# Kernel optimization log

Measured on AMD Instinct MI355X. Metric: run time of the kernel, lower is better.

The kernel has to match this reference:

```python
import jax, jax.numpy as jnp
import numpy as np

B, K, W, H = 32, 64, 100, 150
ALPHA = 0.2        # leaky-relu slope
THRES = 2e-4       # causal threshold


def setup_inputs() -> dict:
    ks = jax.random.split(jax.random.key(0), 20)
    s = 0.1
    inp = {
        "x": jax.random.normal(ks[0], (B, K, W), jnp.float32),
        "y": jax.random.normal(ks[1], (B, K, 1), jnp.float32),
        "z_noise": jax.random.normal(ks[2], (B, H), jnp.float32),
        "lin_w": jax.random.normal(ks[3], (W, W), jnp.float32) * s,
        "lin_b": jax.random.normal(ks[4], (W,), jnp.float32) * s,
        "a": jax.random.normal(ks[5], (2, 1), jnp.float32),
        "bias": jax.random.normal(ks[6], (K, K * W), jnp.float32) * 0.01,
        "gl_wih": jax.random.normal(ks[7], (3 * H, W), jnp.float32) * s,
        "gl_whh": jax.random.normal(ks[8], (3 * H, H), jnp.float32) * s,
        "gl_bih": jax.random.normal(ks[9], (3 * H,), jnp.float32) * s,
        "gl_bhh": jax.random.normal(ks[10], (3 * H,), jnp.float32) * s,
        "mu_w": jax.random.normal(ks[11], (H, H), jnp.float32) * s,
        "mu_b": jax.random.normal(ks[12], (H,), jnp.float32) * s,
        "std_w": jax.random.normal(ks[13], (H, H), jnp.float32) * s,
        "std_b": jax.random.normal(ks[14], (H,), jnp.float32) * s,
        "net_wih": jax.random.normal(ks[15], (K, 3 * H, W), jnp.float32) * s,
        "net_whh": jax.random.normal(ks[16], (K, 3 * H, H), jnp.float32) * s,
        "net_bih": jax.random.normal(ks[17], (K, 3 * H), jnp.float32) * s,
        "net_bhh": jax.random.normal(ks[18], (K, 3 * H), jnp.float32) * s,
    }
    return inp


def _gru_last(wih, whh, bih, bhh, xs, h0):
    # xs: [B, S, in], h0: [B, H] -> final hidden [B, H]. PyTorch gate order r,z,n.
    gx = jnp.einsum('bsi,gi->sbg', xs, wih) + bih  # [S, B, 3H]
    h_dim = h0.shape[-1]

    def step(h, g):
        gh = h @ whh.T + bhh
        r = jax.nn.sigmoid(g[:, :h_dim] + gh[:, :h_dim])
        z = jax.nn.sigmoid(g[:, h_dim:2 * h_dim] + gh[:, h_dim:2 * h_dim])
        n = jnp.tanh(g[:, 2 * h_dim:] + r * gh[:, 2 * h_dim:])
        return (1.0 - z) * n + z * h, None

    h_last, _ = jax.lax.scan(step, h0, gx)
    return h_last


def reference(x, y, z_noise, lin_w, lin_b, a, bias, gl_wih, gl_whh, gl_bih, gl_bhh,
              mu_w, mu_b, std_w, std_b, net_wih, net_whh, net_bih, net_bhh):
    xw = x[:, :, -W:]
    Wx = xw @ lin_w.T + lin_b                       # [B, K, W]
    v = Wx.reshape(Wx.shape[0], K * W)              # [B, K*W]
    # e = a_input @ a, where a_input[...,0]=y broadcast, a_input[...,1]=v tiled per node
    e = a[0, 0] * y + a[1, 0] * v[:, None, :] + bias  # [B, K, K*W]
    e = jax.nn.leaky_relu(e, ALPHA)
    attention = jax.nn.softmax(e, axis=2)           # dropout p=0 -> identity
    A = attention >= THRES                           # [B, K, K*W] mask
    Ax = jnp.where(A, v[:, None, :], 0.0)
    cause_x = Wx + Ax.sum(axis=2, keepdims=True)    # [B, K, W]
    # left GRU over the node dimension (seq len = K)
    h0 = jnp.zeros((cause_x.shape[0], H), cause_x.dtype)
    h_t = _gru_last(gl_wih, gl_whh, gl_bih, gl_bhh, cause_x, h0)  # [B, H]
    mu = h_t @ mu_w.T + mu_b
    log_var = h_t @ std_w.T + std_b
    sigma = jnp.exp(0.5 * log_var)
    z = mu + sigma * z_noise                        # [B, H]
    # K independent GRUs, same input Wx and same init state z -> vmap over weights
    causes = jax.vmap(lambda wi, wh, bi, bh: _gru_last(wi, wh, bi, bh, Wx, z))(
        net_wih, net_whh, net_bih, net_bhh)         # [K, B, H]
    return causes.transpose(1, 0, 2)                # [B, K, H]
```

## Files before the change

### kernel.cpp

```cpp
#include <hip/hip_runtime.h>

#define Bc 32
#define Kc 64
#define Wc 100
#define Hc 150
#define H3c 450
#define KWc 6400
#define ALPHAc 0.2f
#define THRESc 0.0002f

typedef unsigned int u32;
typedef unsigned short u16;
typedef __attribute__((ext_vector_type(8))) short short8;
typedef __attribute__((ext_vector_type(4))) float floatx4;

#define OFF_WX      0u
#define OFF_CS      204800u
#define OFF_GX      206848u
#define OFF_HT      1128448u
#define OFF_Z       1133248u

__device__ __forceinline__ float us2f(u16 u){ u32 x=((u32)u)<<16; return __uint_as_float(x); }
__device__ __forceinline__ u16 f2us(float f){
  u32 x = __float_as_uint(f);
  u32 r = (x + 0x7fffu + ((x>>16)&1u)) >> 16;
  return (u16)r;
}

__global__ void wx_kernel(const float* __restrict__ x, const float* __restrict__ lin_w,
                          const float* __restrict__ lin_b, float* __restrict__ ws){
  int o = blockIdx.x*256 + threadIdx.x;
  if (o >= Bc*KWc) return;
  int i = o % Wc;
  int bk = o / Wc;
  const float4* xr = (const float4*)(x + bk*Wc);
  const float4* wr = (const float4*)(lin_w + i*Wc);
  float acc = lin_b[i];
  #pragma unroll
  for (int j=0;j<25;j++){
    float4 xv = xr[j], wv = wr[j];
    acc += xv.x*wv.x + xv.y*wv.y + xv.z*wv.z + xv.w*wv.w;
  }
  ws[OFF_WX + o] = acc;
}

__global__ void attn_kernel(const float* __restrict__ y, const float* __restrict__ a,
                            const float* __restrict__ bias, float* __restrict__ ws){
  __shared__ float e_l[KWc];
  __shared__ float red[4];
  int row = blockIdx.x;
  int b = row >> 6, k = row & 63;
  int tid = threadIdx.x;
  float a0 = a[0], a1 = a[1];
  float yv = y[row];
  const float* v = ws + OFF_WX + b*KWc;
  const float* br = bias + k*KWc;
  float m = -3.4e38f;
  for (int j=tid; j<KWc; j+=256){
    float e = a0*yv + a1*v[j] + br[j];
    e = (e >= 0.f) ? e : ALPHAc*e;
    e_l[j] = e;
    m = fmaxf(m, e);
  }
  for (int o=32;o;o>>=1) m = fmaxf(m, __shfl_down(m, o));
  if ((tid&63)==0) red[tid>>6] = m;
  __syncthreads();
  m = fmaxf(fmaxf(red[0],red[1]), fmaxf(red[2],red[3]));
  __syncthreads();
  float ssum = 0.f;
  for (int j=tid; j<KWc; j+=256){
    float ex = expf(e_l[j]-m);
    e_l[j] = ex;
    ssum += ex;
  }
  for (int o=32;o;o>>=1) ssum += __shfl_down(ssum, o);
  if ((tid&63)==0) red[tid>>6] = ssum;
  __syncthreads();
  float s = red[0]+red[1]+red[2]+red[3];
  __syncthreads();
  float cs = 0.f;
  for (int j=tid; j<KWc; j+=256){
    float att = e_l[j] / s;
    if (att >= THRESc) cs += v[j];
  }
  for (int o=32;o;o>>=1) cs += __shfl_down(cs, o);
  if ((tid&63)==0) red[tid>>6] = cs;
  __syncthreads();
  if (tid==0) ws[OFF_CS + row] = red[0]+red[1]+red[2]+red[3];
}

__global__ void glproj_kernel(const float* __restrict__ gl_wih, const float* __restrict__ gl_bih,
                              float* __restrict__ ws){
  int o = blockIdx.x*256 + threadIdx.x;
  if (o >= Kc*Bc*H3c) return;
  int g = o % H3c;
  int t = o / H3c;
  int b = t & 31, s = t >> 5;
  float cs = ws[OFF_CS + b*Kc + s];
  const float4* xr = (const float4*)(ws + OFF_WX + b*KWc + s*Wc);
  const float4* wr = (const float4*)(gl_wih + g*Wc);
  float acc = gl_bih[g];
  #pragma unroll
  for (int j=0;j<25;j++){
    float4 wv = wr[j], xv = xr[j];
    acc += (xv.x+cs)*wv.x + (xv.y+cs)*wv.y + (xv.z+cs)*wv.z + (xv.w+cs)*wv.w;
  }
  ws[OFF_GX + o] = acc;
}

__global__ void __launch_bounds__(512,1) glgru4_kernel(
    const float* __restrict__ gl_whh, const float* __restrict__ gl_bhh,
    float* __restrict__ ws){
  __shared__ __align__(16) u16 bF[10*16*40];
  __shared__ float g_l[480*10];
  int b0 = blockIdx.x*8;
  int tid = threadIdx.x;
  int w = tid >> 6, lane = tid & 63, quad = lane >> 4, n16 = lane & 15;

  short8 whhA[4][5];
  #pragma unroll
  for (int ti=0; ti<4; ti++){
    int tile = w*4 + ti;
    int sec = tile/10;
    int sr = (tile - sec*10)*16 + n16;
    bool rowok = (tile < 30) && (sr < Hc);
    int grow = sec*Hc + sr;
    #pragma unroll
    for (int c=0;c<5;c++){
      union { short8 v; u16 u[8]; } t8;
      #pragma unroll
      for (int j=0;j<8;j++){
        int k = c*32 + quad*8 + j;
        float v = (rowok && k < Hc) ? gl_whh[(size_t)grow*Hc + k] : 0.f;
        t8.u[j] = f2us(v);
      }
      whhA[ti][c] = t8.v;
    }
  }
  for (int i=tid; i<10*16*40/2; i+=512) ((u32*)bF)[i] = 0u;

  float hst[3] = {0.f,0.f,0.f};
  float bh_r[3], bh_z[3], bh_n[3];
  int tT[3], tBL[3];
  #pragma unroll
  for (int q=0;q<3;q++){
    int task = tid + q*512;
    if (task < 1200){
      int bl = task/150, t = task - bl*150;
      tT[q] = t; tBL[q] = bl;
      bh_r[q] = gl_bhh[t];
      bh_z[q] = gl_bhh[Hc+t];
      bh_n[q] = gl_bhh[2*Hc+t];
    } else { tT[q] = 0; tBL[q] = -1; }
  }

  for (int s=0;s<Kc;s++){
    __syncthreads();
    float gxr[3], gxz[3], gxn[3];
    const float* gxb = ws + OFF_GX + (size_t)(s*Bc)*H3c;
    #pragma unroll
    for (int q=0;q<3;q++){
      if (tBL[q] >= 0){
        const float* gp = gxb + (size_t)(b0+tBL[q])*H3c;
        int t = tT[q];
        gxr[q] = gp[t]; gxz[q] = gp[Hc+t]; gxn[q] = gp[2*Hc+t];
      }
    }
    const u16* bBase = bF + (size_t)n16*40 + (size_t)quad*8;
    short8 bh[10];
    #pragma unroll
    for (int c=0;c<10;c++) bh[c] = *(const short8*)(bBase + (size_t)c*640);
    floatx4 acc[4] = {{0.f,0.f,0.f,0.f},{0.f,0.f,0.f,0.f},{0.f,0.f,0.f,0.f},{0.f,0.f,0.f,0.f}};
    #pragma unroll
    for (int c=0;c<10;c++){
      int ca = (c<5)? c : (c-5);
      #pragma unroll
      for (int ti=0;ti<4;ti++)
        acc[ti] = __builtin_amdgcn_mfma_f32_16x16x32_bf16(whhA[ti][ca], bh[c], acc[ti], 0,0,0);
    }
    if (n16 < 8){
      #pragma unroll
      for (int ti=0;ti<4;ti++){
        int tile = w*4 + ti;
        if (tile < 30){
          int row0 = tile*16 + quad*4;
          float* gp = g_l + row0*10 + n16;
          #pragma unroll
          for (int r=0;r<4;r++) gp[r*10] = acc[ti][r];
        }
      }
    }
    __syncthreads();
    #pragma unroll
    for (int q=0;q<3;q++){
      if (tBL[q] >= 0){
        int t = tT[q], bl = tBL[q];
        float a_r = gxr[q] + g_l[t*10+bl] + bh_r[q];
        float a_z = gxz[q] + g_l[(160+t)*10+bl] + bh_z[q];
        float r  = 1.f/(1.f+__expf(-a_r));
        float zz = 1.f/(1.f+__expf(-a_z));
        float nx = gxn[q] + r*(g_l[(320+t)*10+bl] + bh_n[q]);
        nx = fminf(fmaxf(nx,-15.f),15.f);
        float e2 = __expf(2.f*nx);
        float n = (e2-1.f)/(e2+1.f);
        float h = (1.f-zz)*n + zz*hst[q];
        hst[q] = h;
        u16 hi = f2us(h); float hif = us2f(hi); u16 lo = f2us(h - hif);
        bF[(t>>5)*640 + bl*40 + (t&31)] = hi;
        bF[(5+(t>>5))*640 + bl*40 + (t&31)] = lo;
      }
    }
  }
  #pragma unroll
  for (int q=0;q<3;q++){
    if (tBL[q] >= 0)
      ws[OFF_HT + (size_t)(b0+tBL[q])*Hc + tT[q]] = hst[q];
  }
}

__global__ void z_kernel(const float* __restrict__ z_noise, const float* __restrict__ mu_w,
                         const float* __restrict__ mu_b, const float* __restrict__ std_w,
                         const float* __restrict__ std_b, float* __restrict__ ws){
  int o = blockIdx.x*256 + threadIdx.x;
  if (o >= Bc*Hc) return;
  int t = o % Hc, b = o / Hc;
  const float* h = ws + OFF_HT + b*Hc;
  const float2* mwr = (const float2*)(mu_w + t*Hc);
  const float2* swr = (const float2*)(std_w + t*Hc);
  float mu = mu_b[t], lv = std_b[t];
  for (int j=0;j<Hc/2;j++){
    float2 mw = mwr[j], sw = swr[j];
    float h0 = h[2*j], h1 = h[2*j+1];
    mu += h0*mw.x + h1*mw.y;
    lv += h0*sw.x + h1*sw.y;
  }
  float sg = expf(0.5f*lv);
  ws[OFF_Z + o] = mu + sg*z_noise[o];
}

__global__ void __launch_bounds__(512,1) causes3_kernel(
    const float* __restrict__ net_wih, const float* __restrict__ net_whh,
    const float* __restrict__ net_bih, const float* __restrict__ net_bhh,
    const float* __restrict__ ws, float* __restrict__ out){
  __shared__ __align__(16) u16 bF[14*16*40];
  __shared__ float g_rz[320*10];
  __shared__ float g_nh[160*10];
  __shared__ float g_np[160*10];
  int kk = blockIdx.x & 63, bg = blockIdx.x >> 6, b0 = bg*8;
  int tid = threadIdx.x;
  int w = tid >> 6, lane = tid & 63, quad = lane >> 4, n16 = lane & 15;
  const float* whhk = net_whh + (size_t)kk*H3c*Hc;
  const float* wihk = net_wih + (size_t)kk*H3c*Wc;
  const float* bihk = net_bih + kk*H3c;
  const float* bhhk = net_bhh + kk*H3c;

  short8 whhA[4][5], wihA[4][4];
  #pragma unroll
  for (int ti=0; ti<4; ti++){
    int tile = w*4 + ti;
    int sec = tile/10;
    int sr = (tile - sec*10)*16 + n16;
    bool rowok = (tile < 30) && (sr < Hc);
    int grow = sec*Hc + sr;
    #pragma unroll
    for (int c=0;c<5;c++){
      union { short8 v; u16 u[8]; } t8;
      #pragma unroll
      for (int j=0;j<8;j++){
        int k = c*32 + quad*8 + j;
        float v = (rowok && k < Hc) ? whhk[(size_t)grow*Hc + k] : 0.f;
        t8.u[j] = f2us(v);
      }
      whhA[ti][c] = t8.v;
    }
    #pragma unroll
    for (int c=0;c<4;c++){
      union { short8 v; u16 u[8]; } t8;
      #pragma unroll
      for (int j=0;j<8;j++){
        int k = c*32 + quad*8 + j;
        float v = (rowok && k < Wc) ? wihk[(size_t)grow*Wc + k] : 0.f;
        t8.u[j] = f2us(v);
      }
      wihA[ti][c] = t8.v;
    }
  }

  for (int i=tid; i<14*16*40/2; i+=512) ((u32*)bF)[i] = 0u;

  float hst[3] = {0.f,0.f,0.f};
  float brz_r[3], brz_z[3], bnh_[3], bnp_[3];
  #pragma unroll
  for (int q=0;q<3;q++){
    int task = tid + q*512;
    if (task < 1200){
      int t = task >> 3, bb = task & 7;
      float h = ws[OFF_Z + (b0+bb)*Hc + t];
      hst[q] = h;
      brz_r[q] = bhhk[t]      + bihk[t];
      brz_z[q] = bhhk[Hc+t]   + bihk[Hc+t];
      bnh_[q]  = bhhk[2*Hc+t];
      bnp_[q]  = bihk[2*Hc+t];
      u16 hi = f2us(h); float hif = us2f(hi); u16 lo = f2us(h - hif);
      bF[(t>>5)*640 + bb*40 + (t&31)] = hi;
      bF[(5+(t>>5))*640 + bb*40 + (t&31)] = lo;
    }
  }
  for (int it=tid; it<800; it+=512){
    int bb = it/100, i = it - bb*100;
    float xv = ws[OFF_WX + (b0+bb)*KWc + i];
    bF[(10+(i>>5))*640 + bb*40 + (i&31)] = f2us(xv);
  }

  int bb0 = tid/100, i0 = tid - bb0*100;
  int it1 = tid + 512;
  int bb1 = it1/100, i1 = it1 - bb1*100;
  bool v1ok = (it1 < 800);

  const bool isN = (w >= 5);
  for (int s=0;s<Kc;s++){
    float xp0 = 0.f, xp1 = 0.f;
    if (s < Kc-1){
      xp0 = ws[OFF_WX + (size_t)(b0+bb0)*KWc + (s+1)*Wc + i0];
      if (v1ok) xp1 = ws[OFF_WX + (size_t)(b0+bb1)*KWc + (s+1)*Wc + i1];
    }
    __syncthreads();
    const u16* bBase = bF + (size_t)n16*40 + (size_t)quad*8;
    short8 bx[4];
    #pragma unroll
    for (int c=0;c<4;c++) bx[c] = *(const short8*)(bBase + (size_t)(10+c)*640);
    floatx4 acc[4] = {{0.f,0.f,0.f,0.f},{0.f,0.f,0.f,0.f},{0.f,0.f,0.f,0.f},{0.f,0.f,0.f,0.f}};
    #pragma unroll
    for (int ca=0;ca<4;ca++){
      #pragma unroll
      for (int ti=0;ti<4;ti++)
        acc[ti] = __builtin_amdgcn_mfma_f32_16x16x32_bf16(wihA[ti][ca], bx[ca], acc[ti], 0,0,0);
    }
    short8 bh[10];
    #pragma unroll
    for (int c=0;c<10;c++) bh[c] = *(const short8*)(bBase + (size_t)c*640);
    if (isN){
      if (n16 < 8){
        #pragma unroll
        for (int ti=0;ti<4;ti++){
          int tile = w*4 + ti;
          if (tile < 30){
            int srb = (tile - 20)*16 + quad*4;
            float* gq = g_np + srb*10 + n16;
            #pragma unroll
            for (int r=0;r<4;r++) gq[r*10] = acc[ti][r];
          }
        }
      }
      #pragma unroll
      for (int ti=0;ti<4;ti++) acc[ti] = (floatx4){0.f,0.f,0.f,0.f};
    }
    #pragma unroll
    for (int c=0;c<10;c++){
      int ca = (c<5)? c : (c-5);
      #pragma unroll
      for (int ti=0;ti<4;ti++)
        acc[ti] = __builtin_amdgcn_mfma_f32_16x16x32_bf16(whhA[ti][ca], bh[c], acc[ti], 0,0,0);
    }
    if (n16 < 8){
      #pragma unroll
      for (int ti=0;ti<4;ti++){
        int tile = w*4 + ti;
        if (tile < 30){
          int sec = tile/10;
          int srb = (tile - sec*10)*16 + quad*4;
          if (sec < 2){
            float* gp = g_rz + (sec*160 + srb)*10 + n16;
            #pragma unroll
            for (int r=0;r<4;r++) gp[r*10] = acc[ti][r];
          } else {
            float* gh = g_nh + srb*10 + n16;
            #pragma unroll
            for (int r=0;r<4;r++) gh[r*10] = acc[ti][r];
          }
        }
      }
    }
    __syncthreads();
    #pragma unroll
    for (int q=0;q<3;q++){
      int task = tid + q*512;
      if (task < 1200){
        int t = task >> 3, bb = task & 7;
        float a_r = g_rz[t*10+bb] + brz_r[q];
        float a_z = g_rz[(160+t)*10+bb] + brz_z[q];
        float r  = 1.f/(1.f+__expf(-a_r));
        float zz = 1.f/(1.f+__expf(-a_z));
        float nx = (g_np[t*10+bb] + bnp_[q]) + r*(g_nh[t*10+bb] + bnh_[q]);
        nx = fminf(fmaxf(nx,-15.f),15.f);
        float e2 = __expf(2.f*nx);
        float n = (e2-1.f)/(e2+1.f);
        float h = (1.f-zz)*n + zz*hst[q];
        hst[q] = h;
        u16 hi = f2us(h); float hif = us2f(hi); u16 lo = f2us(h - hif);
        bF[(t>>5)*640 + bb*40 + (t&31)] = hi;
        bF[(5+(t>>5))*640 + bb*40 + (t&31)] = lo;
      }
    }
    if (s < Kc-1){
      bF[(10+(i0>>5))*640 + bb0*40 + (i0&31)] = f2us(xp0);
      if (v1ok) bF[(10+(i1>>5))*640 + bb1*40 + (i1&31)] = f2us(xp1);
    }
  }
  #pragma unroll
  for (int q=0;q<3;q++){
    int task = tid + q*512;
    if (task < 1200){
      int t = task >> 3, bb = task & 7;
      out[((size_t)(b0+bb)*Kc + kk)*Hc + t] = hst[q];
    }
  }
}

extern "C" void kernel_launch(void* const* d_in, const int* in_sizes, int n_in,
                              void* d_out, int out_size, void* d_ws, size_t ws_size,
                              hipStream_t stream){
  const float* x        = (const float*)d_in[0];
  const float* y        = (const float*)d_in[1];
  const float* z_noise  = (const float*)d_in[2];
  const float* lin_w    = (const float*)d_in[3];
  const float* lin_b    = (const float*)d_in[4];
  const float* a        = (const float*)d_in[5];
  const float* bias     = (const float*)d_in[6];
  const float* gl_wih   = (const float*)d_in[7];
  const float* gl_whh   = (const float*)d_in[8];
  const float* gl_bih   = (const float*)d_in[9];
  const float* gl_bhh   = (const float*)d_in[10];
  const float* mu_w     = (const float*)d_in[11];
  const float* mu_b     = (const float*)d_in[12];
  const float* std_w    = (const float*)d_in[13];
  const float* std_b    = (const float*)d_in[14];
  const float* net_wih  = (const float*)d_in[15];
  const float* net_whh  = (const float*)d_in[16];
  const float* net_bih  = (const float*)d_in[17];
  const float* net_bhh  = (const float*)d_in[18];
  float* ws = (float*)d_ws;
  float* out = (float*)d_out;

  wx_kernel<<<(Bc*KWc+255)/256, 256, 0, stream>>>(x, lin_w, lin_b, ws);
  attn_kernel<<<Bc*Kc, 256, 0, stream>>>(y, a, bias, ws);
  glproj_kernel<<<(Kc*Bc*H3c+255)/256, 256, 0, stream>>>(gl_wih, gl_bih, ws);
  glgru4_kernel<<<4, 512, 0, stream>>>(gl_whh, gl_bhh, ws);
  z_kernel<<<(Bc*Hc+255)/256, 256, 0, stream>>>(z_noise, mu_w, mu_b, std_w, std_b, ws);
  causes3_kernel<<<Kc*4, 512, 0, stream>>>(net_wih, net_whh, net_bih, net_bhh, ws, out);
}
```

Before: 516.6 us.

## Vectorize attention softmax, use log-space threshold, batch LDS reads in GRU steps

The attention kernel now reads inputs as float4, uses fast __expf, and compares logits against m+log(THRES*s) instead of dividing every element, which drops one LDS write pass and a barrier. Weight loads into the MFMA fragments use float2 reads, and the GRU gate updates first gather all shared-memory values and then compute, to expose more memory-level parallelism. In the net GRU loop the load of the next input is moved after the barrier. The log-space threshold and __expf can flip mask decisions for values near the threshold.

```diff
diff --git a/kernel.cpp b/kernel.cpp
--- a/kernel.cpp
+++ b/kernel.cpp
@@ -46,21 +46,27 @@
 
 __global__ void attn_kernel(const float* __restrict__ y, const float* __restrict__ a,
                             const float* __restrict__ bias, float* __restrict__ ws){
-  __shared__ float e_l[KWc];
+  __shared__ __align__(16) float e_l[KWc];
   __shared__ float red[4];
   int row = blockIdx.x;
   int b = row >> 6, k = row & 63;
   int tid = threadIdx.x;
   float a0 = a[0], a1 = a[1];
   float yv = y[row];
-  const float* v = ws + OFF_WX + b*KWc;
-  const float* br = bias + k*KWc;
+  const float4* v4  = (const float4*)(ws + OFF_WX + (size_t)b*KWc);
+  const float4* br4 = (const float4*)(bias + (size_t)k*KWc);
+  float4* e4 = (float4*)e_l;
+  float ay = a0*yv;
   float m = -3.4e38f;
-  for (int j=tid; j<KWc; j+=256){
-    float e = a0*yv + a1*v[j] + br[j];
-    e = (e >= 0.f) ? e : ALPHAc*e;
-    e_l[j] = e;
-    m = fmaxf(m, e);
+  for (int j=tid; j<KWc/4; j+=256){
+    float4 vv = v4[j], bb = br4[j];
+    float4 e;
+    e.x = ay + a1*vv.x + bb.x; e.x = (e.x>=0.f)?e.x:ALPHAc*e.x;
+    e.y = ay + a1*vv.y + bb.y; e.y = (e.y>=0.f)?e.y:ALPHAc*e.y;
+    e.z = ay + a1*vv.z + bb.z; e.z = (e.z>=0.f)?e.z:ALPHAc*e.z;
+    e.w = ay + a1*vv.w + bb.w; e.w = (e.w>=0.f)?e.w:ALPHAc*e.w;
+    e4[j] = e;
+    m = fmaxf(m, fmaxf(fmaxf(e.x,e.y), fmaxf(e.z,e.w)));
   }
   for (int o=32;o;o>>=1) m = fmaxf(m, __shfl_down(m, o));
   if ((tid&63)==0) red[tid>>6] = m;
@@ -68,20 +74,23 @@
   m = fmaxf(fmaxf(red[0],red[1]), fmaxf(red[2],red[3]));
   __syncthreads();
   float ssum = 0.f;
-  for (int j=tid; j<KWc; j+=256){
-    float ex = expf(e_l[j]-m);
-    e_l[j] = ex;
-    ssum += ex;
+  for (int j=tid; j<KWc/4; j+=256){
+    float4 e = e4[j];
+    ssum += __expf(e.x-m) + __expf(e.y-m) + __expf(e.z-m) + __expf(e.w-m);
   }
   for (int o=32;o;o>>=1) ssum += __shfl_down(ssum, o);
   if ((tid&63)==0) red[tid>>6] = ssum;
   __syncthreads();
   float s = red[0]+red[1]+red[2]+red[3];
-  __syncthreads();
+  float thr = m + logf(THRESc * s);
   float cs = 0.f;
-  for (int j=tid; j<KWc; j+=256){
-    float att = e_l[j] / s;
-    if (att >= THRESc) cs += v[j];
+  for (int j=tid; j<KWc/4; j+=256){
+    float4 e = e4[j];
+    float4 vv = v4[j];
+    if (e.x >= thr) cs += vv.x;
+    if (e.y >= thr) cs += vv.y;
+    if (e.z >= thr) cs += vv.z;
+    if (e.w >= thr) cs += vv.w;
   }
   for (int o=32;o;o>>=1) cs += __shfl_down(cs, o);
   if ((tid&63)==0) red[tid>>6] = cs;
@@ -125,14 +134,16 @@
     int sr = (tile - sec*10)*16 + n16;
     bool rowok = (tile < 30) && (sr < Hc);
     int grow = sec*Hc + sr;
+    const float* wr = gl_whh + (size_t)grow*Hc;
     #pragma unroll
     for (int c=0;c<5;c++){
       union { short8 v; u16 u[8]; } t8;
       #pragma unroll
-      for (int j=0;j<8;j++){
-        int k = c*32 + quad*8 + j;
-        float v = (rowok && k < Hc) ? gl_whh[(size_t)grow*Hc + k] : 0.f;
-        t8.u[j] = f2us(v);
+      for (int j2=0;j2<4;j2++){
+        int kk2 = c*32 + quad*8 + j2*2;
+        float2 wv = (rowok && (kk2+1) < Hc) ? *(const float2*)(wr + kk2) : make_float2(0.f,0.f);
+        t8.u[j2*2]   = f2us(wv.x);
+        t8.u[j2*2+1] = f2us(wv.y);
       }
       whhA[ti][c] = t8.v;
     }
@@ -191,15 +202,25 @@
       }
     }
     __syncthreads();
+    float grv[3], gzv[3], gnv[3];
     #pragma unroll
     for (int q=0;q<3;q++){
       if (tBL[q] >= 0){
         int t = tT[q], bl = tBL[q];
-        float a_r = gxr[q] + g_l[t*10+bl] + bh_r[q];
-        float a_z = gxz[q] + g_l[(160+t)*10+bl] + bh_z[q];
+        grv[q] = g_l[t*10+bl];
+        gzv[q] = g_l[(160+t)*10+bl];
+        gnv[q] = g_l[(320+t)*10+bl];
+      }
+    }
+    #pragma unroll
+    for (int q=0;q<3;q++){
+      if (tBL[q] >= 0){
+        int t = tT[q], bl = tBL[q];
+        float a_r = gxr[q] + grv[q] + bh_r[q];
+        float a_z = gxz[q] + gzv[q] + bh_z[q];
         float r  = 1.f/(1.f+__expf(-a_r));
         float zz = 1.f/(1.f+__expf(-a_z));
-        float nx = gxn[q] + r*(g_l[(320+t)*10+bl] + bh_n[q]);
+        float nx = gxn[q] + r*(gnv[q] + bh_n[q]);
         nx = fminf(fmaxf(nx,-15.f),15.f);
         float e2 = __expf(2.f*nx);
         float n = (e2-1.f)/(e2+1.f);
@@ -262,25 +283,29 @@
     int sr = (tile - sec*10)*16 + n16;
     bool rowok = (tile < 30) && (sr < Hc);
     int grow = sec*Hc + sr;
+    const float* wr = whhk + (size_t)grow*Hc;
     #pragma unroll
     for (int c=0;c<5;c++){
       union { short8 v; u16 u[8]; } t8;
       #pragma unroll
-      for (int j=0;j<8;j++){
-        int k = c*32 + quad*8 + j;
-        float v = (rowok && k < Hc) ? whhk[(size_t)grow*Hc + k] : 0.f;
-        t8.u[j] = f2us(v);
+      for (int j2=0;j2<4;j2++){
+        int kk2 = c*32 + quad*8 + j2*2;
+        float2 wv = (rowok && (kk2+1) < Hc) ? *(const float2*)(wr + kk2) : make_float2(0.f,0.f);
+        t8.u[j2*2]   = f2us(wv.x);
+        t8.u[j2*2+1] = f2us(wv.y);
       }
       whhA[ti][c] = t8.v;
     }
+    const float* wr2 = wihk + (size_t)grow*Wc;
     #pragma unroll
     for (int c=0;c<4;c++){
       union { short8 v; u16 u[8]; } t8;
       #pragma unroll
-      for (int j=0;j<8;j++){
-        int k = c*32 + quad*8 + j;
-        float v = (rowok && k < Wc) ? wihk[(size_t)grow*Wc + k] : 0.f;
-        t8.u[j] = f2us(v);
+      for (int j2=0;j2<4;j2++){
+        int kk2 = c*32 + quad*8 + j2*2;
+        float2 wv = (rowok && (kk2+1) < Wc) ? *(const float2*)(wr2 + kk2) : make_float2(0.f,0.f);
+        t8.u[j2*2]   = f2us(wv.x);
+        t8.u[j2*2+1] = f2us(wv.y);
       }
       wihA[ti][c] = t8.v;
     }
@@ -319,12 +344,12 @@
 
   const bool isN = (w >= 5);
   for (int s=0;s<Kc;s++){
+    __syncthreads();
     float xp0 = 0.f, xp1 = 0.f;
     if (s < Kc-1){
       xp0 = ws[OFF_WX + (size_t)(b0+bb0)*KWc + (s+1)*Wc + i0];
       if (v1ok) xp1 = ws[OFF_WX + (size_t)(b0+bb1)*KWc + (s+1)*Wc + i1];
     }
-    __syncthreads();
     const u16* bBase = bF + (size_t)n16*40 + (size_t)quad*8;
     short8 bx[4];
     #pragma unroll
@@ -382,16 +407,28 @@
       }
     }
     __syncthreads();
+    float grv[3], gzv[3], gnpv[3], gnhv[3];
     #pragma unroll
     for (int q=0;q<3;q++){
       int task = tid + q*512;
       if (task < 1200){
         int t = task >> 3, bb = task & 7;
-        float a_r = g_rz[t*10+bb] + brz_r[q];
-        float a_z = g_rz[(160+t)*10+bb] + brz_z[q];
+        grv[q]  = g_rz[t*10+bb];
+        gzv[q]  = g_rz[(160+t)*10+bb];
+        gnpv[q] = g_np[t*10+bb];
+        gnhv[q] = g_nh[t*10+bb];
+      }
+    }
+    #pragma unroll
+    for (int q=0;q<3;q++){
+      int task = tid + q*512;
+      if (task < 1200){
+        int t = task >> 3, bb = task & 7;
+        float a_r = grv[q] + brz_r[q];
+        float a_z = gzv[q] + brz_z[q];
         float r  = 1.f/(1.f+__expf(-a_r));
         float zz = 1.f/(1.f+__expf(-a_z));
-        float nx = (g_np[t*10+bb] + bnp_[q]) + r*(g_nh[t*10+bb] + bnh_[q]);
+        float nx = (gnpv[q] + bnp_[q]) + r*(gnhv[q] + bnh_[q]);
         nx = fminf(fmaxf(nx,-15.f),15.f);
         float e2 = __expf(2.f*nx);
         float n = (e2-1.f)/(e2+1.f);
```

Result: slower. 562.9 us (+9.0%).
